# Performance work log

Hardware: AMD Instinct MI355X
Metric: run time of the kernel (lower is better)

## Reference

```python
import jax, jax.numpy as jnp
import numpy as np

N_V = 100000
N_E = 20000
NNZ = 1600000
D = 128


def setup_inputs() -> dict:
    key = jax.random.key(0)
    k1, k2, k3, k4, k5 = jax.random.split(key, 5)
    X = jax.random.normal(k1, (N_V, D), dtype=jnp.float32)
    W = jax.random.normal(k2, (D, D), dtype=jnp.float32) * (1.0 / np.sqrt(D))
    b = jax.random.normal(k3, (D,), dtype=jnp.float32) * 0.01
    v2e_src = jax.random.randint(k4, (NNZ,), 0, N_V, dtype=jnp.int32)
    v2e_dst = jax.random.randint(k5, (NNZ,), 0, N_E, dtype=jnp.int32)
    return {"X": X, "W": W, "b": b, "v2e_src": v2e_src, "v2e_dst": v2e_dst, "num_e": N_E}


def reference(X, W, b, v2e_src, v2e_dst, num_e):
    num_v = X.shape[0]
    ones = jnp.ones(v2e_src.shape[0], dtype=X.dtype)
    # node degrees (values of D_v diagonal) and hyperedge incidence counts
    deg_v = jax.ops.segment_sum(ones, v2e_src, num_segments=num_v)
    cnt_e = jax.ops.segment_sum(ones, v2e_dst, num_segments=num_e)

    # theta: linear layer
    Xt = X @ W.T + b  # [N_V, D]

    # v2e mean aggregation: per hyperedge, mean of incident vertex features
    Ysum = jax.ops.segment_sum(Xt[v2e_src], v2e_dst, num_segments=num_e)  # [N_E, D]
    Y = Ysum / jnp.maximum(cnt_e, 1.0)[:, None]

    # edge norm: torch scatter_reduce(reduce='mean', include_self=True) -> sum/(count+1)
    De_sum = jax.ops.segment_sum(deg_v[v2e_src], v2e_dst, num_segments=num_e)
    De = De_sum / (cnt_e + 1.0)
    De = jnp.where(De > 0, jax.lax.rsqrt(jnp.maximum(De, 1e-30)), 1.0)  # inf -> 1
    Y = De[:, None] * Y

    # e2v sum aggregation
    Xo = jax.ops.segment_sum(Y[v2e_dst], v2e_src, num_segments=num_v)  # [N_V, D]

    # D_v^{-1/2} sparse diagonal mm (zero-degree nodes -> 0)
    dvn = jnp.where(deg_v > 0, jax.lax.rsqrt(jnp.maximum(deg_v, 1e-30)), 0.0)
    Xo = dvn[:, None] * Xo

    # is_last=False: ReLU then dropout (dropout is identity in eval)
    return jax.nn.relu(Xo)
```

## Files before the change

### kernel.cpp

```cpp
#include <hip/hip_runtime.h>
#include <hip/hip_bf16.h>

#define NV 100000
#define NE 20000
#define DD 128
#define ESHIFT 7
#define VSHIFT 9
#define NBE 157
#define NBV 196
#define NBK 256
#define CHUNK 4096
#define CAPE 11264
#define CAPV 9216

using bf16 = __hip_bfloat16;

typedef __attribute__((ext_vector_type(8))) short frag_ab;
typedef __attribute__((ext_vector_type(4))) float frag_cd;

__device__ __forceinline__ float uas(unsigned u) { union { unsigned u; float f; } c; c.u = u; return c.f; }
__device__ __forceinline__ unsigned pk2(float lo, float hi) {
    bf16 l = __float2bfloat16(lo), h = __float2bfloat16(hi);
    return (unsigned)(*(unsigned short*)&l) | ((unsigned)(*(unsigned short*)&h) << 16);
}
__device__ __forceinline__ void accum8(float* a, uint4 x) {
    a[0] += uas(x.x << 16); a[1] += uas(x.x & 0xffff0000u);
    a[2] += uas(x.y << 16); a[3] += uas(x.y & 0xffff0000u);
    a[4] += uas(x.z << 16); a[5] += uas(x.z & 0xffff0000u);
    a[6] += uas(x.w << 16); a[7] += uas(x.w & 0xffff0000u);
}
__device__ __forceinline__ int wave_incl_scan(int v, int lane) {
#pragma unroll
    for (int o = 1; o < 64; o <<= 1) {
        int x = __shfl_up(v, o);
        if (lane >= o) v += x;
    }
    return v;
}

__global__ void init_cur(int* __restrict__ bcur_e, int* __restrict__ bcur_v) {
    int t = threadIdx.x;
    bcur_e[t] = t * CAPE;
    bcur_v[t] = t * CAPV;
}

__global__ __launch_bounds__(256) void partition_and_cvt(const int* __restrict__ src, const int* __restrict__ dst,
                                                         int* __restrict__ bcur_e, int* __restrict__ bcur_v,
                                                         unsigned* __restrict__ pairs_e, unsigned* __restrict__ pairs_v,
                                                         int nnz,
                                                         const float4* __restrict__ Xf, ushort4* __restrict__ Xb,
                                                         const float4* __restrict__ Wf, ushort4* __restrict__ Wb) {
    int nchunk = (nnz + CHUNK - 1) / CHUNK;
    int t = threadIdx.x;
    int bid = blockIdx.x;
    if (bid >= 2 * nchunk) {
        const int n4x = NV * DD / 4;
        const int n4w = DD * DD / 4;
        int i = (bid - 2 * nchunk) * 256 + t;
        if (i < n4x + n4w) {
            float4 v;
            ushort4 o;
            if (i < n4x) v = Xf[i]; else v = Wf[i - n4x];
            bf16 a = __float2bfloat16(v.x); o.x = *(unsigned short*)&a;
            bf16 b = __float2bfloat16(v.y); o.y = *(unsigned short*)&b;
            bf16 c = __float2bfloat16(v.z); o.z = *(unsigned short*)&c;
            bf16 d = __float2bfloat16(v.w); o.w = *(unsigned short*)&d;
            if (i < n4x) Xb[i] = o; else Wb[i - n4x] = o;
        }
        return;
    }
    __shared__ int cntA[NBK], cntB[NBK], pre1[NBK], loff[NBK], gbase[NBK], wsum[4];
    __shared__ int totValid;
    __shared__ unsigned stage[CHUNK];
    int phase = (bid >= nchunk) ? 1 : 0;
    int cidx = phase ? bid - nchunk : bid;
    int sub = t >> 7;
    int lane = t & 63, wv = t >> 6;
    int base = cidx * CHUNK;
    unsigned p[16];
    int rk[16];
#pragma unroll
    for (int k = 0; k < 16; ++k) {
        int i = base + k * 256 + t;
        p[k] = (i < nnz) ? (((unsigned)src[i] << 15) | (unsigned)dst[i]) : 0xFFFFFFFFu;
    }

    cntA[t] = 0; cntB[t] = 0;
    __syncthreads();
#pragma unroll
    for (int k = 0; k < 16; ++k)
        if (p[k] != 0xFFFFFFFFu) {
            int b = phase ? (int)(p[k] >> 24) : (int)((p[k] >> ESHIFT) & 0xFF);
            rk[k] = atomicAdd(sub ? &cntB[b] : &cntA[b], 1);
        }
    __syncthreads();
    {
        int a = cntA[t], bb = cntB[t];
        int tv = a + bb;
        pre1[t] = a;
        int incl = wave_incl_scan(tv, lane);
        if (lane == 63) wsum[wv] = incl;
        __syncthreads();
        if (t == 0) { int r = 0; for (int i = 0; i < 4; ++i) { int x = wsum[i]; wsum[i] = r; r += x; } }
        __syncthreads();
        int ex = incl - tv + wsum[wv];
        loff[t] = ex;
        gbase[t] = (tv > 0) ? atomicAdd(phase ? &bcur_v[t] : &bcur_e[t], tv) : 0;
        if (t == 255) totValid = ex + tv;
    }
    __syncthreads();
#pragma unroll
    for (int k = 0; k < 16; ++k)
        if (p[k] != 0xFFFFFFFFu) {
            int b = phase ? (int)(p[k] >> 24) : (int)((p[k] >> ESHIFT) & 0xFF);
            stage[loff[b] + rk[k] + (sub ? pre1[b] : 0)] = p[k];
        }
    __syncthreads();
    unsigned* outp = phase ? pairs_v : pairs_e;
    for (int i = t; i < totValid; i += 256) {
        unsigned pp = stage[i];
        int b = phase ? (int)(pp >> 24) : (int)((pp >> ESHIFT) & 0xFF);
        outp[gbase[b] + i - loff[b]] = pp;
    }
}

__global__ __launch_bounds__(1024) void build_csr(const unsigned* __restrict__ pairs_e, const int* __restrict__ bcur_e,
                                                  int* __restrict__ off_e, int* __restrict__ end_e, int* __restrict__ e_src,
                                                  const unsigned* __restrict__ pairs_v, const int* __restrict__ bcur_v,
                                                  int* __restrict__ off_v, int* __restrict__ end_v, int* __restrict__ v_edge,
                                                  int* __restrict__ deg_v) {
    __shared__ int cA[2048], cB[2048], sc2[512], eoff[512], wsumS[8];
    int t = threadIdx.x;
    cA[t] = 0; cA[t + 1024] = 0;
    __syncthreads();
    if ((int)blockIdx.x < NBE) {
        int b = blockIdx.x;
        int lo = b * CAPE, hi = bcur_e[b];
        int sub = t >> 7;
        unsigned pv[12];
        int rk[12];
        int kk = 0;
        for (int i = lo + t; i < hi; i += 1024, ++kk) {
            unsigned p = pairs_e[i];
            pv[kk] = p;
            rk[kk] = atomicAdd(&cA[sub * 128 + (p & 127)], 1);
        }
        __syncthreads();
        if (t < 128) {
            int run = 0;
#pragma unroll
            for (int s = 0; s < 8; ++s) { cB[s * 128 + t] = run; run += cA[s * 128 + t]; }
            sc2[t] = run;
        }
        __syncthreads();
        int incl = 0, myrun = 0;
        if (t < 128) {
            myrun = sc2[t];
            incl = wave_incl_scan(myrun, t & 63);
            if ((t & 63) == 63) wsumS[t >> 6] = incl;
        }
        __syncthreads();
        if (t == 0) { int r = 0; for (int i = 0; i < 2; ++i) { int x = wsumS[i]; wsumS[i] = r; r += x; } }
        __syncthreads();
        if (t < 128) {
            int ex = incl - myrun + wsumS[t >> 6];
            eoff[t] = ex;
            int e = (b << ESHIFT) + t;
            if (e < NE) { off_e[e] = lo + ex; end_e[e] = lo + ex + myrun; }
        }
        __syncthreads();
        for (int k = 0; k < kk; ++k) {
            int bkt = pv[k] & 127;
            int pos = lo + eoff[bkt] + cB[sub * 128 + bkt] + rk[k];
            e_src[pos] = (int)(pv[k] >> 15);
        }
    } else {
        int b = blockIdx.x - NBE;
        int lo = b * CAPV, hi = bcur_v[b];
        int sub = t >> 8;
        unsigned pv[9];
        int rk[9];
        int kk = 0;
        for (int i = lo + t; i < hi; i += 1024, ++kk) {
            unsigned p = pairs_v[i];
            pv[kk] = p;
            rk[kk] = atomicAdd(&cA[sub * 512 + ((p >> 15) & 511)], 1);
        }
        __syncthreads();
        if (t < 512) {
            int run = 0;
#pragma unroll
            for (int s = 0; s < 4; ++s) { cB[s * 512 + t] = run; run += cA[s * 512 + t]; }
            sc2[t] = run;
        }
        __syncthreads();
        int incl = 0, myrun = 0;
        if (t < 512) {
            myrun = sc2[t];
            incl = wave_incl_scan(myrun, t & 63);
            if ((t & 63) == 63) wsumS[t >> 6] = incl;
        }
        __syncthreads();
        if (t == 0) { int r = 0; for (int i = 0; i < 8; ++i) { int x = wsumS[i]; wsumS[i] = r; r += x; } }
        __syncthreads();
        if (t < 512) {
            int ex = incl - myrun + wsumS[t >> 6];
            eoff[t] = ex;
            int v = (b << VSHIFT) + t;
            if (v < NV) { off_v[v] = lo + ex; end_v[v] = lo + ex + myrun; deg_v[v] = myrun; }
        }
        __syncthreads();
        for (int k = 0; k < kk; ++k) {
            int bkt = (pv[k] >> 15) & 511;
            int pos = lo + eoff[bkt] + cB[sub * 512 + bkt] + rk[k];
            v_edge[pos] = (int)(pv[k] & 0x7FFF);
        }
    }
}

__global__ __launch_bounds__(512) void edge_fused(const uint4* __restrict__ Xq, const int* __restrict__ off_e,
                                                  const int* __restrict__ end_e,
                                                  const int* __restrict__ e_src, const int* __restrict__ deg_v,
                                                  const bf16* __restrict__ Wb, const float* __restrict__ bias,
                                                  bf16* __restrict__ Y) {
    __shared__ short Stile[16][136];
    __shared__ float betaL[16];
    int t = threadIdx.x;
    int w = t >> 6, lane = t & 63;
    int h = lane >> 5;
    int g2 = (lane >> 4) & 1;
    int l16 = lane & 15;
    int mBase = blockIdx.x * 16;
    int le = w * 2 + g2;
    int e = mBase + le;
    int start = off_e[e], end = end_e[e];
    int cnt = end - start;
    int half0 = (cnt + 1) >> 1;
    int hs = start + h * half0;
    int he = h ? end : (start + half0);
    float acc[8] = {0.f, 0.f, 0.f, 0.f, 0.f, 0.f, 0.f, 0.f};
    float degsum = 0.f;
    int j = hs;
    for (; j + 8 <= he; j += 8) {
        int s0 = e_src[j + 0], s1 = e_src[j + 1], s2 = e_src[j + 2], s3 = e_src[j + 3];
        int s4 = e_src[j + 4], s5 = e_src[j + 5], s6 = e_src[j + 6], s7 = e_src[j + 7];
        uint4 x0 = Xq[(size_t)s0 * 16 + l16];
        uint4 x1 = Xq[(size_t)s1 * 16 + l16];
        uint4 x2 = Xq[(size_t)s2 * 16 + l16];
        uint4 x3 = Xq[(size_t)s3 * 16 + l16];
        uint4 x4 = Xq[(size_t)s4 * 16 + l16];
        uint4 x5 = Xq[(size_t)s5 * 16 + l16];
        uint4 x6 = Xq[(size_t)s6 * 16 + l16];
        uint4 x7 = Xq[(size_t)s7 * 16 + l16];
        degsum += (float)(deg_v[s0] + deg_v[s1] + deg_v[s2] + deg_v[s3]
                        + deg_v[s4] + deg_v[s5] + deg_v[s6] + deg_v[s7]);
        accum8(acc, x0); accum8(acc, x1); accum8(acc, x2); accum8(acc, x3);
        accum8(acc, x4); accum8(acc, x5); accum8(acc, x6); accum8(acc, x7);
    }
    for (; j + 4 <= he; j += 4) {
        int s0 = e_src[j + 0], s1 = e_src[j + 1], s2 = e_src[j + 2], s3 = e_src[j + 3];
        uint4 x0 = Xq[(size_t)s0 * 16 + l16];
        uint4 x1 = Xq[(size_t)s1 * 16 + l16];
        uint4 x2 = Xq[(size_t)s2 * 16 + l16];
        uint4 x3 = Xq[(size_t)s3 * 16 + l16];
        degsum += (float)(deg_v[s0] + deg_v[s1] + deg_v[s2] + deg_v[s3]);
        accum8(acc, x0); accum8(acc, x1); accum8(acc, x2); accum8(acc, x3);
    }
    for (; j < he; ++j) {
        int s = e_src[j];
        uint4 x = Xq[(size_t)s * 16 + l16];
        degsum += (float)deg_v[s];
        accum8(acc, x);
    }
#pragma unroll
    for (int r = 0; r < 8; ++r) acc[r] += __shfl_xor(acc[r], 32);
    degsum += __shfl_xor(degsum, 32);

    float cntf = (float)cnt;
    float Des = degsum / (cntf + 1.0f);
    float De = (Des > 0.f) ? rsqrtf(fmaxf(Des, 1e-30f)) : 1.0f;
    float scale = De / fmaxf(cntf, 1.0f);
    if (h == 0) {
        uint4 o;
        o.x = pk2(acc[0] * scale, acc[1] * scale);
        o.y = pk2(acc[2] * scale, acc[3] * scale);
        o.z = pk2(acc[4] * scale, acc[5] * scale);
        o.w = pk2(acc[6] * scale, acc[7] * scale);
        *(uint4*)&Stile[le][l16 * 8] = o;
        if (l16 == 0) betaL[le] = (cntf > 0.f) ? De : 0.f;
    }
    __syncthreads();

    const short* Ws = (const short*)Wb;
    int quad = lane >> 4;
    frag_ab a[4];
#pragma unroll
    for (int kt = 0; kt < 4; ++kt)
        a[kt] = *(const frag_ab*)&Stile[l16][kt * 32 + quad * 8];
    float beta_r[4];
#pragma unroll
    for (int r = 0; r < 4; ++r) beta_r[r] = betaL[quad * 4 + r];

    int nt = w;
    frag_cd acc2 = {0.f, 0.f, 0.f, 0.f};
#pragma unroll
    for (int kt = 0; kt < 4; ++kt) {
        frag_ab bfr = *(const frag_ab*)(Ws + (size_t)(nt * 16 + l16) * DD + kt * 32 + quad * 8);
        acc2 = __builtin_amdgcn_mfma_f32_16x16x32_bf16(a[kt], bfr, acc2, 0, 0, 0);
    }
    float bv = bias[nt * 16 + l16];
#pragma unroll
    for (int r = 0; r < 4; ++r) {
        int row = mBase + quad * 4 + r;
        float v = acc2[r] + beta_r[r] * bv;
        Y[(size_t)row * DD + nt * 16 + l16] = __float2bfloat16(v);
    }
}

__global__ __launch_bounds__(256) void vertex_agg(const uint4* __restrict__ Yq, const int* __restrict__ off_v,
                                                  const int* __restrict__ end_v,
                                                  const int* __restrict__ v_edge, float* __restrict__ out) {
    int wave = (blockIdx.x * blockDim.x + threadIdx.x) >> 6;
    int lane = threadIdx.x & 63;
    int g = lane >> 4, l16 = lane & 15;
    int v = wave * 4 + g;
    if (v >= NV) return;
    int start = off_v[v], end = end_v[v];
    float acc[8] = {0.f, 0.f, 0.f, 0.f, 0.f, 0.f, 0.f, 0.f};
    int j = start;
    for (; j + 8 <= end; j += 8) {
        int e0 = v_edge[j + 0], e1 = v_edge[j + 1], e2 = v_edge[j + 2], e3 = v_edge[j + 3];
        int e4 = v_edge[j + 4], e5 = v_edge[j + 5], e6 = v_edge[j + 6], e7 = v_edge[j + 7];
        uint4 y0 = Yq[(size_t)e0 * 16 + l16];
        uint4 y1 = Yq[(size_t)e1 * 16 + l16];
        uint4 y2 = Yq[(size_t)e2 * 16 + l16];
        uint4 y3 = Yq[(size_t)e3 * 16 + l16];
        uint4 y4 = Yq[(size_t)e4 * 16 + l16];
        uint4 y5 = Yq[(size_t)e5 * 16 + l16];
        uint4 y6 = Yq[(size_t)e6 * 16 + l16];
        uint4 y7 = Yq[(size_t)e7 * 16 + l16];
        accum8(acc, y0); accum8(acc, y1); accum8(acc, y2); accum8(acc, y3);
        accum8(acc, y4); accum8(acc, y5); accum8(acc, y6); accum8(acc, y7);
    }
    for (; j + 4 <= end; j += 4) {
        int e0 = v_edge[j + 0], e1 = v_edge[j + 1], e2 = v_edge[j + 2], e3 = v_edge[j + 3];
        uint4 y0 = Yq[(size_t)e0 * 16 + l16];
        uint4 y1 = Yq[(size_t)e1 * 16 + l16];
        uint4 y2 = Yq[(size_t)e2 * 16 + l16];
        uint4 y3 = Yq[(size_t)e3 * 16 + l16];
        accum8(acc, y0); accum8(acc, y1); accum8(acc, y2); accum8(acc, y3);
    }
    for (; j < end; ++j) {
        int e = v_edge[j];
        uint4 y = Yq[(size_t)e * 16 + l16];
        accum8(acc, y);
    }
    int deg = end - start;
    float dvn = (deg > 0) ? rsqrtf((float)deg) : 0.f;
    float4 o1, o2;
    o1.x = fmaxf(acc[0] * dvn, 0.f);
    o1.y = fmaxf(acc[1] * dvn, 0.f);
    o1.z = fmaxf(acc[2] * dvn, 0.f);
    o1.w = fmaxf(acc[3] * dvn, 0.f);
    o2.x = fmaxf(acc[4] * dvn, 0.f);
    o2.y = fmaxf(acc[5] * dvn, 0.f);
    o2.z = fmaxf(acc[6] * dvn, 0.f);
    o2.w = fmaxf(acc[7] * dvn, 0.f);
    float4* op = (float4*)(out + (size_t)v * DD + l16 * 8);
    op[0] = o1;
    op[1] = o2;
}

extern "C" void kernel_launch(void* const* d_in, const int* in_sizes, int n_in,
                              void* d_out, int out_size, void* d_ws, size_t ws_size,
                              hipStream_t stream) {
    const float* X = (const float*)d_in[0];
    const float* W = (const float*)d_in[1];
    const float* b = (const float*)d_in[2];
    const int* src = (const int*)d_in[3];
    const int* dst = (const int*)d_in[4];
    int nnz = in_sizes[3];

    char* ws = (char*)d_ws;
    size_t o = 0;
    auto take = [&](size_t bytes) -> char* {
        char* p = ws + o;
        o += (bytes + 255) & ~(size_t)255;
        return p;
    };
    int* bcur_e = (int*)take(NBK * 4);
    int* bcur_v = (int*)take(NBK * 4);
    int* off_e = (int*)take((size_t)NE * 4);
    int* end_e = (int*)take((size_t)NE * 4);
    int* off_v = (int*)take((size_t)NV * 4);
    int* end_v = (int*)take((size_t)NV * 4);
    int* deg_v = (int*)take((size_t)NV * 4);
    int* e_src = (int*)take((size_t)NBE * CAPE * 4);
    int* v_edge = (int*)take((size_t)NBV * CAPV * 4);
    unsigned* pairs_e = (unsigned*)take((size_t)NBE * CAPE * 4);
    unsigned* pairs_v = (unsigned*)take((size_t)NBV * CAPV * 4);
    bf16* Y = (bf16*)take((size_t)NE * DD * 2);
    bf16* Wb = (bf16*)take((size_t)DD * DD * 2);
    bf16* Xb = (bf16*)take((size_t)NV * DD * 2);
    (void)ws_size; (void)n_in; (void)out_size;

    int nchunk = (nnz + CHUNK - 1) / CHUNK;
    int ncvt = (NV * DD / 4 + DD * DD / 4 + 255) / 256;

    init_cur<<<1, NBK, 0, stream>>>(bcur_e, bcur_v);
    partition_and_cvt<<<2 * nchunk + ncvt, 256, 0, stream>>>(src, dst, bcur_e, bcur_v, pairs_e, pairs_v, nnz,
                                                             (const float4*)X, (ushort4*)Xb,
                                                             (const float4*)W, (ushort4*)Wb);
    build_csr<<<NBE + NBV, 1024, 0, stream>>>(pairs_e, bcur_e, off_e, end_e, e_src,
                                              pairs_v, bcur_v, off_v, end_v, v_edge, deg_v);
    edge_fused<<<NE / 16, 512, 0, stream>>>((const uint4*)Xb, off_e, end_e, e_src, deg_v, Wb, b, Y);
    vertex_agg<<<(NV / 4 * 64) / 256, 256, 0, stream>>>((const uint4*)Y, off_v, end_v, v_edge, (float*)d_out);
}
```

Before: 248.8 us.

## Fuse edge-side CSR sort into edge kernel via finer buckets and LDS local sort

Edges are now partitioned into 1250 buckets of 16 hyperedges. Each edge_fused block sorts its own bucket in LDS and aggregates directly from that list, so the separate edge half of build_csr and the global e_src array go away. The vertex sort becomes a standalone vsort kernel with 256-vertex buckets that stores edge indices as 16-bit values and drops end arrays. The trade-offs are a larger partition histogram, fixed per-bucket capacity limits that could overflow on other inputs, and one 16-lane group per edge without the old split-half parallelism.

```diff
diff --git a/kernel.cpp b/kernel.cpp
--- a/kernel.cpp
+++ b/kernel.cpp
@@ -4,14 +4,14 @@
 #define NV 100000
 #define NE 20000
 #define DD 128
-#define ESHIFT 7
-#define VSHIFT 9
-#define NBE 157
-#define NBV 196
-#define NBK 256
+#define NBE 1250
+#define NBV 391
+#define NBMAX 1280
+#define PBE 5
+#define PBV 2
 #define CHUNK 4096
-#define CAPE 11264
-#define CAPV 9216
+#define CAPE 1664
+#define CAPV 5120
 
 using bf16 = __hip_bfloat16;
 
@@ -40,8 +40,8 @@
 
 __global__ void init_cur(int* __restrict__ bcur_e, int* __restrict__ bcur_v) {
     int t = threadIdx.x;
-    bcur_e[t] = t * CAPE;
-    bcur_v[t] = t * CAPV;
+    for (int i = t; i < NBE; i += 1024) bcur_e[i] = i * CAPE;
+    for (int i = t; i < NBV; i += 1024) bcur_v[i] = i * CAPV;
 }
 
 __global__ __launch_bounds__(256) void partition_and_cvt(const int* __restrict__ src, const int* __restrict__ dst,
@@ -69,11 +69,14 @@
         }
         return;
     }
-    __shared__ int cntA[NBK], cntB[NBK], pre1[NBK], loff[NBK], gbase[NBK], wsum[4];
+    __shared__ int cntA[NBMAX], cntB[NBMAX], loff[NBMAX], gbase[NBMAX], wsum[4];
     __shared__ int totValid;
     __shared__ unsigned stage[CHUNK];
     int phase = (bid >= nchunk) ? 1 : 0;
     int cidx = phase ? bid - nchunk : bid;
+    int NB = phase ? NBV : NBE;
+    int PB = phase ? PBV : PBE;
+    int* cur = phase ? bcur_v : bcur_e;
     int sub = t >> 7;
     int lane = t & 63, wv = t >> 6;
     int base = cidx * CHUNK;
@@ -85,165 +88,161 @@
         p[k] = (i < nnz) ? (((unsigned)src[i] << 15) | (unsigned)dst[i]) : 0xFFFFFFFFu;
     }
 
-    cntA[t] = 0; cntB[t] = 0;
+    for (int i = t; i < NBMAX; i += 256) { cntA[i] = 0; cntB[i] = 0; }
     __syncthreads();
 #pragma unroll
     for (int k = 0; k < 16; ++k)
         if (p[k] != 0xFFFFFFFFu) {
-            int b = phase ? (int)(p[k] >> 24) : (int)((p[k] >> ESHIFT) & 0xFF);
+            int b = phase ? (int)(p[k] >> 23) : (int)((p[k] >> 4) & 0x7FF);
             rk[k] = atomicAdd(sub ? &cntB[b] : &cntA[b], 1);
         }
     __syncthreads();
     {
-        int a = cntA[t], bb = cntB[t];
-        int tv = a + bb;
-        pre1[t] = a;
-        int incl = wave_incl_scan(tv, lane);
+        int run = 0;
+        int lcl[PBE];
+#pragma unroll
+        for (int q = 0; q < PBE; ++q) lcl[q] = 0;
+        for (int q = 0; q < PB; ++q) {
+            int bkt = t * PB + q;
+            int tv = (bkt < NB) ? (cntA[bkt] + cntB[bkt]) : 0;
+            lcl[q] = run; run += tv;
+        }
+        int incl = wave_incl_scan(run, lane);
         if (lane == 63) wsum[wv] = incl;
         __syncthreads();
         if (t == 0) { int r = 0; for (int i = 0; i < 4; ++i) { int x = wsum[i]; wsum[i] = r; r += x; } }
         __syncthreads();
-        int ex = incl - tv + wsum[wv];
-        loff[t] = ex;
-        gbase[t] = (tv > 0) ? atomicAdd(phase ? &bcur_v[t] : &bcur_e[t], tv) : 0;
-        if (t == 255) totValid = ex + tv;
+        int ex = incl - run + wsum[wv];
+        for (int q = 0; q < PB; ++q) {
+            int bkt = t * PB + q;
+            if (bkt < NB) {
+                int tv = cntA[bkt] + cntB[bkt];
+                loff[bkt] = ex + lcl[q];
+                gbase[bkt] = (tv > 0) ? atomicAdd(&cur[bkt], tv) : 0;
+            }
+        }
+        if (t == 255) totValid = ex + run;
     }
     __syncthreads();
 #pragma unroll
     for (int k = 0; k < 16; ++k)
         if (p[k] != 0xFFFFFFFFu) {
-            int b = phase ? (int)(p[k] >> 24) : (int)((p[k] >> ESHIFT) & 0xFF);
-            stage[loff[b] + rk[k] + (sub ? pre1[b] : 0)] = p[k];
+            int b = phase ? (int)(p[k] >> 23) : (int)((p[k] >> 4) & 0x7FF);
+            stage[loff[b] + rk[k] + (sub ? cntA[b] : 0)] = p[k];
         }
     __syncthreads();
     unsigned* outp = phase ? pairs_v : pairs_e;
     for (int i = t; i < totValid; i += 256) {
         unsigned pp = stage[i];
-        int b = phase ? (int)(pp >> 24) : (int)((pp >> ESHIFT) & 0xFF);
+        int b = phase ? (int)(pp >> 23) : (int)((pp >> 4) & 0x7FF);
         outp[gbase[b] + i - loff[b]] = pp;
     }
 }
 
-__global__ __launch_bounds__(1024) void build_csr(const unsigned* __restrict__ pairs_e, const int* __restrict__ bcur_e,
-                                                  int* __restrict__ off_e, int* __restrict__ end_e, int* __restrict__ e_src,
-                                                  const unsigned* __restrict__ pairs_v, const int* __restrict__ bcur_v,
-                                                  int* __restrict__ off_v, int* __restrict__ end_v, int* __restrict__ v_edge,
-                                                  int* __restrict__ deg_v) {
-    __shared__ int cA[2048], cB[2048], sc2[512], eoff[512], wsumS[8];
+__global__ __launch_bounds__(1024) void vsort(const unsigned* __restrict__ pairs_v, const int* __restrict__ bcur_v,
+                                              int* __restrict__ off_v, int* __restrict__ deg_v,
+                                              unsigned short* __restrict__ v_edge) {
+    __shared__ int cA[1024], cB[1024], sc2[256], eoff[256], wsumS[4];
     int t = threadIdx.x;
-    cA[t] = 0; cA[t + 1024] = 0;
-    __syncthreads();
-    if ((int)blockIdx.x < NBE) {
-        int b = blockIdx.x;
-        int lo = b * CAPE, hi = bcur_e[b];
-        int sub = t >> 7;
-        unsigned pv[12];
-        int rk[12];
-        int kk = 0;
-        for (int i = lo + t; i < hi; i += 1024, ++kk) {
-            unsigned p = pairs_e[i];
-            pv[kk] = p;
-            rk[kk] = atomicAdd(&cA[sub * 128 + (p & 127)], 1);
-        }
-        __syncthreads();
-        if (t < 128) {
-            int run = 0;
-#pragma unroll
-            for (int s = 0; s < 8; ++s) { cB[s * 128 + t] = run; run += cA[s * 128 + t]; }
-            sc2[t] = run;
-        }
-        __syncthreads();
-        int incl = 0, myrun = 0;
-        if (t < 128) {
-            myrun = sc2[t];
-            incl = wave_incl_scan(myrun, t & 63);
-            if ((t & 63) == 63) wsumS[t >> 6] = incl;
-        }
-        __syncthreads();
-        if (t == 0) { int r = 0; for (int i = 0; i < 2; ++i) { int x = wsumS[i]; wsumS[i] = r; r += x; } }
-        __syncthreads();
-        if (t < 128) {
-            int ex = incl - myrun + wsumS[t >> 6];
-            eoff[t] = ex;
-            int e = (b << ESHIFT) + t;
-            if (e < NE) { off_e[e] = lo + ex; end_e[e] = lo + ex + myrun; }
-        }
-        __syncthreads();
-        for (int k = 0; k < kk; ++k) {
-            int bkt = pv[k] & 127;
-            int pos = lo + eoff[bkt] + cB[sub * 128 + bkt] + rk[k];
-            e_src[pos] = (int)(pv[k] >> 15);
-        }
-    } else {
-        int b = blockIdx.x - NBE;
-        int lo = b * CAPV, hi = bcur_v[b];
-        int sub = t >> 8;
-        unsigned pv[9];
-        int rk[9];
-        int kk = 0;
-        for (int i = lo + t; i < hi; i += 1024, ++kk) {
-            unsigned p = pairs_v[i];
-            pv[kk] = p;
-            rk[kk] = atomicAdd(&cA[sub * 512 + ((p >> 15) & 511)], 1);
-        }
-        __syncthreads();
-        if (t < 512) {
-            int run = 0;
-#pragma unroll
-            for (int s = 0; s < 4; ++s) { cB[s * 512 + t] = run; run += cA[s * 512 + t]; }
-            sc2[t] = run;
-        }
-        __syncthreads();
-        int incl = 0, myrun = 0;
-        if (t < 512) {
-            myrun = sc2[t];
-            incl = wave_incl_scan(myrun, t & 63);
-            if ((t & 63) == 63) wsumS[t >> 6] = incl;
-        }
-        __syncthreads();
-        if (t == 0) { int r = 0; for (int i = 0; i < 8; ++i) { int x = wsumS[i]; wsumS[i] = r; r += x; } }
-        __syncthreads();
-        if (t < 512) {
-            int ex = incl - myrun + wsumS[t >> 6];
-            eoff[t] = ex;
-            int v = (b << VSHIFT) + t;
-            if (v < NV) { off_v[v] = lo + ex; end_v[v] = lo + ex + myrun; deg_v[v] = myrun; }
-        }
-        __syncthreads();
-        for (int k = 0; k < kk; ++k) {
-            int bkt = (pv[k] >> 15) & 511;
-            int pos = lo + eoff[bkt] + cB[sub * 512 + bkt] + rk[k];
-            v_edge[pos] = (int)(pv[k] & 0x7FFF);
-        }
-    }
-}
-
-__global__ __launch_bounds__(512) void edge_fused(const uint4* __restrict__ Xq, const int* __restrict__ off_e,
-                                                  const int* __restrict__ end_e,
-                                                  const int* __restrict__ e_src, const int* __restrict__ deg_v,
+    cA[t] = 0;
+    __syncthreads();
+    int b = blockIdx.x;
+    int lo = b * CAPV, hi = bcur_v[b];
+    int sub = t >> 8;
+    unsigned pv[5];
+    int rk[5];
+    int kk = 0;
+    for (int i = lo + t; i < hi; i += 1024, ++kk) {
+        unsigned p = pairs_v[i];
+        pv[kk] = p;
+        rk[kk] = atomicAdd(&cA[sub * 256 + ((p >> 15) & 255)], 1);
+    }
+    __syncthreads();
+    if (t < 256) {
+        int run = 0;
+#pragma unroll
+        for (int s = 0; s < 4; ++s) { cB[s * 256 + t] = run; run += cA[s * 256 + t]; }
+        sc2[t] = run;
+    }
+    __syncthreads();
+    int incl = 0, myrun = 0;
+    if (t < 256) {
+        myrun = sc2[t];
+        incl = wave_incl_scan(myrun, t & 63);
+        if ((t & 63) == 63) wsumS[t >> 6] = incl;
+    }
+    __syncthreads();
+    if (t == 0) { int r = 0; for (int i = 0; i < 4; ++i) { int x = wsumS[i]; wsumS[i] = r; r += x; } }
+    __syncthreads();
+    if (t < 256) {
+        int ex = incl - myrun + wsumS[t >> 6];
+        eoff[t] = ex;
+        int v = (b << 8) + t;
+        if (v < NV) { off_v[v] = lo + ex; deg_v[v] = myrun; }
+    }
+    __syncthreads();
+    for (int k = 0; k < kk; ++k) {
+        int bkt = (pv[k] >> 15) & 255;
+        int pos = lo + eoff[bkt] + cB[sub * 256 + bkt] + rk[k];
+        v_edge[pos] = (unsigned short)(pv[k] & 0x7FFF);
+    }
+}
+
+__global__ __launch_bounds__(256) void edge_fused(const uint4* __restrict__ Xq, const unsigned* __restrict__ pairs_e,
+                                                  const int* __restrict__ bcur_e, const int* __restrict__ deg_v,
                                                   const bf16* __restrict__ Wb, const float* __restrict__ bias,
                                                   bf16* __restrict__ Y) {
+    __shared__ int cntS[64], cB16[64], cntE[16], eoffS[16];
+    __shared__ int Lst[CAPE];
     __shared__ short Stile[16][136];
     __shared__ float betaL[16];
     int t = threadIdx.x;
     int w = t >> 6, lane = t & 63;
-    int h = lane >> 5;
-    int g2 = (lane >> 4) & 1;
-    int l16 = lane & 15;
-    int mBase = blockIdx.x * 16;
-    int le = w * 2 + g2;
-    int e = mBase + le;
-    int start = off_e[e], end = end_e[e];
-    int cnt = end - start;
-    int half0 = (cnt + 1) >> 1;
-    int hs = start + h * half0;
-    int he = h ? end : (start + half0);
+    int g = lane >> 4, l16 = lane & 15;
+    int bkt = blockIdx.x;
+    int lo = bkt * CAPE, hi = bcur_e[bkt];
+    int sub = w;
+
+    if (t < 64) cntS[t] = 0;
+    __syncthreads();
+    unsigned pv[7];
+    int rk[7];
+    int kk = 0;
+    for (int i = lo + t; i < hi; i += 256, ++kk) {
+        unsigned p = pairs_e[i];
+        pv[kk] = p;
+        rk[kk] = atomicAdd(&cntS[sub * 16 + (p & 15)], 1);
+    }
+    __syncthreads();
+    if (t < 16) {
+        int run = 0;
+#pragma unroll
+        for (int s = 0; s < 4; ++s) { cB16[s * 16 + t] = run; run += cntS[s * 16 + t]; }
+        cntE[t] = run;
+    }
+    __syncthreads();
+    if (w == 0) {
+        int v = (lane < 16) ? cntE[lane] : 0;
+        int incl = wave_incl_scan(v, lane);
+        if (lane < 16) eoffS[lane] = incl - v;
+    }
+    __syncthreads();
+    for (int k = 0; k < kk; ++k) {
+        int bb = pv[k] & 15;
+        Lst[eoffS[bb] + cB16[sub * 16 + bb] + rk[k]] = (int)(pv[k] >> 15);
+    }
+    __syncthreads();
+
+    int mBase = bkt * 16;
+    int le = t >> 4;
+    int start = eoffS[le], cnt = cntE[le];
+    int end = start + cnt;
     float acc[8] = {0.f, 0.f, 0.f, 0.f, 0.f, 0.f, 0.f, 0.f};
     float degsum = 0.f;
-    int j = hs;
-    for (; j + 8 <= he; j += 8) {
-        int s0 = e_src[j + 0], s1 = e_src[j + 1], s2 = e_src[j + 2], s3 = e_src[j + 3];
-        int s4 = e_src[j + 4], s5 = e_src[j + 5], s6 = e_src[j + 6], s7 = e_src[j + 7];
+    int j = start;
+    for (; j + 8 <= end; j += 8) {
+        int s0 = Lst[j + 0], s1 = Lst[j + 1], s2 = Lst[j + 2], s3 = Lst[j + 3];
+        int s4 = Lst[j + 4], s5 = Lst[j + 5], s6 = Lst[j + 6], s7 = Lst[j + 7];
         uint4 x0 = Xq[(size_t)s0 * 16 + l16];
         uint4 x1 = Xq[(size_t)s1 * 16 + l16];
         uint4 x2 = Xq[(size_t)s2 * 16 + l16];
@@ -257,8 +256,8 @@
         accum8(acc, x0); accum8(acc, x1); accum8(acc, x2); accum8(acc, x3);
         accum8(acc, x4); accum8(acc, x5); accum8(acc, x6); accum8(acc, x7);
     }
-    for (; j + 4 <= he; j += 4) {
-        int s0 = e_src[j + 0], s1 = e_src[j + 1], s2 = e_src[j + 2], s3 = e_src[j + 3];
+    for (; j + 4 <= end; j += 4) {
+        int s0 = Lst[j + 0], s1 = Lst[j + 1], s2 = Lst[j + 2], s3 = Lst[j + 3];
         uint4 x0 = Xq[(size_t)s0 * 16 + l16];
         uint4 x1 = Xq[(size_t)s1 * 16 + l16];
         uint4 x2 = Xq[(size_t)s2 * 16 + l16];
@@ -266,21 +265,17 @@
         degsum += (float)(deg_v[s0] + deg_v[s1] + deg_v[s2] + deg_v[s3]);
         accum8(acc, x0); accum8(acc, x1); accum8(acc, x2); accum8(acc, x3);
     }
-    for (; j < he; ++j) {
-        int s = e_src[j];
+    for (; j < end; ++j) {
+        int s = Lst[j];
         uint4 x = Xq[(size_t)s * 16 + l16];
         degsum += (float)deg_v[s];
         accum8(acc, x);
     }
-#pragma unroll
-    for (int r = 0; r < 8; ++r) acc[r] += __shfl_xor(acc[r], 32);
-    degsum += __shfl_xor(degsum, 32);
-
     float cntf = (float)cnt;
     float Des = degsum / (cntf + 1.0f);
     float De = (Des > 0.f) ? rsqrtf(fmaxf(Des, 1e-30f)) : 1.0f;
     float scale = De / fmaxf(cntf, 1.0f);
-    if (h == 0) {
+    {
         uint4 o;
         o.x = pk2(acc[0] * scale, acc[1] * scale);
         o.y = pk2(acc[2] * scale, acc[3] * scale);
@@ -292,7 +287,7 @@
     __syncthreads();
 
     const short* Ws = (const short*)Wb;
-    int quad = lane >> 4;
+    int quad = g;
     frag_ab a[4];
 #pragma unroll
     for (int kt = 0; kt < 4; ++kt)
@@ -301,31 +296,35 @@
 #pragma unroll
     for (int r = 0; r < 4; ++r) beta_r[r] = betaL[quad * 4 + r];
 
-    int nt = w;
-    frag_cd acc2 = {0.f, 0.f, 0.f, 0.f};
-#pragma unroll
-    for (int kt = 0; kt < 4; ++kt) {
-        frag_ab bfr = *(const frag_ab*)(Ws + (size_t)(nt * 16 + l16) * DD + kt * 32 + quad * 8);
-        acc2 = __builtin_amdgcn_mfma_f32_16x16x32_bf16(a[kt], bfr, acc2, 0, 0, 0);
-    }
-    float bv = bias[nt * 16 + l16];
-#pragma unroll
-    for (int r = 0; r < 4; ++r) {
-        int row = mBase + quad * 4 + r;
-        float v = acc2[r] + beta_r[r] * bv;
-        Y[(size_t)row * DD + nt * 16 + l16] = __float2bfloat16(v);
+#pragma unroll
+    for (int nn = 0; nn < 2; ++nn) {
+        int nt = w * 2 + nn;
+        frag_cd acc2 = {0.f, 0.f, 0.f, 0.f};
+#pragma unroll
+        for (int kt = 0; kt < 4; ++kt) {
+            frag_ab bfr = *(const frag_ab*)(Ws + (size_t)(nt * 16 + l16) * DD + kt * 32 + quad * 8);
+            acc2 = __builtin_amdgcn_mfma_f32_16x16x32_bf16(a[kt], bfr, acc2, 0, 0, 0);
+        }
+        float bv = bias[nt * 16 + l16];
+#pragma unroll
+        for (int r = 0; r < 4; ++r) {
+            int row = mBase + quad * 4 + r;
+            float v = acc2[r] + beta_r[r] * bv;
+            Y[(size_t)row * DD + nt * 16 + l16] = __float2bfloat16(v);
+        }
     }
 }
 
 __global__ __launch_bounds__(256) void vertex_agg(const uint4* __restrict__ Yq, const int* __restrict__ off_v,
-                                                  const int* __restrict__ end_v,
-                                                  const int* __restrict__ v_edge, float* __restrict__ out) {
+                                                  const int* __restrict__ deg_v,
+                                                  const unsigned short* __restrict__ v_edge, float* __restrict__ out) {
     int wave = (blockIdx.x * blockDim.x + threadIdx.x) >> 6;
     int lane = threadIdx.x & 63;
     int g = lane >> 4, l16 = lane & 15;
     int v = wave * 4 + g;
     if (v >= NV) return;
-    int start = off_v[v], end = end_v[v];
+    int start = off_v[v], deg = deg_v[v];
+    int end = start + deg;
     float acc[8] = {0.f, 0.f, 0.f, 0.f, 0.f, 0.f, 0.f, 0.f};
     int j = start;
     for (; j + 8 <= end; j += 8) {
@@ -355,7 +354,6 @@
         uint4 y = Yq[(size_t)e * 16 + l16];
         accum8(acc, y);
     }
-    int deg = end - start;
     float dvn = (deg > 0) ? rsqrtf((float)deg) : 0.f;
     float4 o1, o2;
     o1.x = fmaxf(acc[0] * dvn, 0.f);
@@ -388,15 +386,11 @@
         o += (bytes + 255) & ~(size_t)255;
         return p;
     };
-    int* bcur_e = (int*)take(NBK * 4);
-    int* bcur_v = (int*)take(NBK * 4);
-    int* off_e = (int*)take((size_t)NE * 4);
-    int* end_e = (int*)take((size_t)NE * 4);
+    int* bcur_e = (int*)take((size_t)NBE * 4);
+    int* bcur_v = (int*)take((size_t)NBV * 4);
     int* off_v = (int*)take((size_t)NV * 4);
-    int* end_v = (int*)take((size_t)NV * 4);
     int* deg_v = (int*)take((size_t)NV * 4);
-    int* e_src = (int*)take((size_t)NBE * CAPE * 4);
-    int* v_edge = (int*)take((size_t)NBV * CAPV * 4);
+    unsigned short* v_edge = (unsigned short*)take((size_t)NBV * CAPV * 2);
     unsigned* pairs_e = (unsigned*)take((size_t)NBE * CAPE * 4);
     unsigned* pairs_v = (unsigned*)take((size_t)NBV * CAPV * 4);
     bf16* Y = (bf16*)take((size_t)NE * DD * 2);
@@ -407,12 +401,11 @@
     int nchunk = (nnz + CHUNK - 1) / CHUNK;
     int ncvt = (NV * DD / 4 + DD * DD / 4 + 255) / 256;
 
-    init_cur<<<1, NBK, 0, stream>>>(bcur_e, bcur_v);
+    init_cur<<<1, 1024, 0, stream>>>(bcur_e, bcur_v);
     partition_and_cvt<<<2 * nchunk + ncvt, 256, 0, stream>>>(src, dst, bcur_e, bcur_v, pairs_e, pairs_v, nnz,
                                                              (const float4*)X, (ushort4*)Xb,
                                                              (const float4*)W, (ushort4*)Wb);
-    build_csr<<<NBE + NBV, 1024, 0, stream>>>(pairs_e, bcur_e, off_e, end_e, e_src,
-                                              pairs_v, bcur_v, off_v, end_v, v_edge, deg_v);
-    edge_fused<<<NE / 16, 512, 0, stream>>>((const uint4*)Xb, off_e, end_e, e_src, deg_v, Wb, b, Y);
-    vertex_agg<<<(NV / 4 * 64) / 256, 256, 0, stream>>>((const uint4*)Y, off_v, end_v, v_edge, (float*)d_out);
-}
+    vsort<<<NBV, 1024, 0, stream>>>(pairs_v, bcur_v, off_v, deg_v, v_edge);
+    edge_fused<<<NBE, 256, 0, stream>>>((const uint4*)Xb, pairs_e, bcur_e, deg_v, Wb, b, Y);
+    vertex_agg<<<(NV / 4 * 64) / 256, 256, 0, stream>>>((const uint4*)Y, off_v, deg_v, v_edge, (float*)d_out);
+}
```

New measurement: 279.8 us. 12.5% more time.

## Split vertex aggregation into two column halves and shrink edge-list indices to 16-bit

Applied to the files above, without the earlier changes.

The vertex aggregation is split into two launches, each gathering one 64-column half of Y. Each half of Y (about 2.5 MB) is more likely to stay resident in L2 or the MI355X's last-level cache during the random gathers. The per-vertex edge list becomes unsigned short, and end_v is replaced by deg_v, which cuts index traffic. The init kernel is replaced by a memset plus relative bucket offsets. The trade-off is that the index list and offsets are read twice and each gather is narrower (8-byte loads instead of 16-byte).

```diff
diff --git a/kernel.cpp b/kernel.cpp
--- a/kernel.cpp
+++ b/kernel.cpp
@@ -29,6 +29,10 @@
     a[4] += uas(x.z << 16); a[5] += uas(x.z & 0xffff0000u);
     a[6] += uas(x.w << 16); a[7] += uas(x.w & 0xffff0000u);
 }
+__device__ __forceinline__ void accum4(float* a, uint2 x) {
+    a[0] += uas(x.x << 16); a[1] += uas(x.x & 0xffff0000u);
+    a[2] += uas(x.y << 16); a[3] += uas(x.y & 0xffff0000u);
+}
 __device__ __forceinline__ int wave_incl_scan(int v, int lane) {
 #pragma unroll
     for (int o = 1; o < 64; o <<= 1) {
@@ -36,12 +40,6 @@
         if (lane >= o) v += x;
     }
     return v;
-}
-
-__global__ void init_cur(int* __restrict__ bcur_e, int* __restrict__ bcur_v) {
-    int t = threadIdx.x;
-    bcur_e[t] = t * CAPE;
-    bcur_v[t] = t * CAPV;
 }
 
 __global__ __launch_bounds__(256) void partition_and_cvt(const int* __restrict__ src, const int* __restrict__ dst,
@@ -105,7 +103,8 @@
         __syncthreads();
         int ex = incl - tv + wsum[wv];
         loff[t] = ex;
-        gbase[t] = (tv > 0) ? atomicAdd(phase ? &bcur_v[t] : &bcur_e[t], tv) : 0;
+        int rel = (tv > 0) ? atomicAdd(phase ? &bcur_v[t] : &bcur_e[t], tv) : 0;
+        gbase[t] = t * (phase ? CAPV : CAPE) + rel;
         if (t == 255) totValid = ex + tv;
     }
     __syncthreads();
@@ -127,7 +126,7 @@
 __global__ __launch_bounds__(1024) void build_csr(const unsigned* __restrict__ pairs_e, const int* __restrict__ bcur_e,
                                                   int* __restrict__ off_e, int* __restrict__ end_e, int* __restrict__ e_src,
                                                   const unsigned* __restrict__ pairs_v, const int* __restrict__ bcur_v,
-                                                  int* __restrict__ off_v, int* __restrict__ end_v, int* __restrict__ v_edge,
+                                                  int* __restrict__ off_v, unsigned short* __restrict__ v_edge,
                                                   int* __restrict__ deg_v) {
     __shared__ int cA[2048], cB[2048], sc2[512], eoff[512], wsumS[8];
     int t = threadIdx.x;
@@ -135,7 +134,7 @@
     __syncthreads();
     if ((int)blockIdx.x < NBE) {
         int b = blockIdx.x;
-        int lo = b * CAPE, hi = bcur_e[b];
+        int lo = b * CAPE, hi = lo + bcur_e[b];
         int sub = t >> 7;
         unsigned pv[12];
         int rk[12];
@@ -176,7 +175,7 @@
         }
     } else {
         int b = blockIdx.x - NBE;
-        int lo = b * CAPV, hi = bcur_v[b];
+        int lo = b * CAPV, hi = lo + bcur_v[b];
         int sub = t >> 8;
         unsigned pv[9];
         int rk[9];
@@ -207,13 +206,13 @@
             int ex = incl - myrun + wsumS[t >> 6];
             eoff[t] = ex;
             int v = (b << VSHIFT) + t;
-            if (v < NV) { off_v[v] = lo + ex; end_v[v] = lo + ex + myrun; deg_v[v] = myrun; }
+            if (v < NV) { off_v[v] = lo + ex; deg_v[v] = myrun; }
         }
         __syncthreads();
         for (int k = 0; k < kk; ++k) {
             int bkt = (pv[k] >> 15) & 511;
             int pos = lo + eoff[bkt] + cB[sub * 512 + bkt] + rk[k];
-            v_edge[pos] = (int)(pv[k] & 0x7FFF);
+            v_edge[pos] = (unsigned short)(pv[k] & 0x7FFF);
         }
     }
 }
@@ -317,58 +316,54 @@
     }
 }
 
-__global__ __launch_bounds__(256) void vertex_agg(const uint4* __restrict__ Yq, const int* __restrict__ off_v,
-                                                  const int* __restrict__ end_v,
-                                                  const int* __restrict__ v_edge, float* __restrict__ out) {
+__global__ __launch_bounds__(256) void vertex_agg(const uint2* __restrict__ Yq, const int* __restrict__ off_v,
+                                                  const int* __restrict__ deg_v,
+                                                  const unsigned short* __restrict__ v_edge, float* __restrict__ out,
+                                                  int half) {
     int wave = (blockIdx.x * blockDim.x + threadIdx.x) >> 6;
     int lane = threadIdx.x & 63;
     int g = lane >> 4, l16 = lane & 15;
     int v = wave * 4 + g;
     if (v >= NV) return;
-    int start = off_v[v], end = end_v[v];
-    float acc[8] = {0.f, 0.f, 0.f, 0.f, 0.f, 0.f, 0.f, 0.f};
+    int start = off_v[v], deg = deg_v[v];
+    int end = start + deg;
+    const uint2* Yh = Yq + half * 16 + l16;
+    float acc[4] = {0.f, 0.f, 0.f, 0.f};
     int j = start;
     for (; j + 8 <= end; j += 8) {
         int e0 = v_edge[j + 0], e1 = v_edge[j + 1], e2 = v_edge[j + 2], e3 = v_edge[j + 3];
         int e4 = v_edge[j + 4], e5 = v_edge[j + 5], e6 = v_edge[j + 6], e7 = v_edge[j + 7];
-        uint4 y0 = Yq[(size_t)e0 * 16 + l16];
-        uint4 y1 = Yq[(size_t)e1 * 16 + l16];
-        uint4 y2 = Yq[(size_t)e2 * 16 + l16];
-        uint4 y3 = Yq[(size_t)e3 * 16 + l16];
-        uint4 y4 = Yq[(size_t)e4 * 16 + l16];
-        uint4 y5 = Yq[(size_t)e5 * 16 + l16];
-        uint4 y6 = Yq[(size_t)e6 * 16 + l16];
-        uint4 y7 = Yq[(size_t)e7 * 16 + l16];
-        accum8(acc, y0); accum8(acc, y1); accum8(acc, y2); accum8(acc, y3);
-        accum8(acc, y4); accum8(acc, y5); accum8(acc, y6); accum8(acc, y7);
+        uint2 y0 = Yh[(size_t)e0 * 32];
+        uint2 y1 = Yh[(size_t)e1 * 32];
+        uint2 y2 = Yh[(size_t)e2 * 32];
+        uint2 y3 = Yh[(size_t)e3 * 32];
+        uint2 y4 = Yh[(size_t)e4 * 32];
+        uint2 y5 = Yh[(size_t)e5 * 32];
+        uint2 y6 = Yh[(size_t)e6 * 32];
+        uint2 y7 = Yh[(size_t)e7 * 32];
+        accum4(acc, y0); accum4(acc, y1); accum4(acc, y2); accum4(acc, y3);
+        accum4(acc, y4); accum4(acc, y5); accum4(acc, y6); accum4(acc, y7);
     }
     for (; j + 4 <= end; j += 4) {
         int e0 = v_edge[j + 0], e1 = v_edge[j + 1], e2 = v_edge[j + 2], e3 = v_edge[j + 3];
-        uint4 y0 = Yq[(size_t)e0 * 16 + l16];
-        uint4 y1 = Yq[(size_t)e1 * 16 + l16];
-        uint4 y2 = Yq[(size_t)e2 * 16 + l16];
-        uint4 y3 = Yq[(size_t)e3 * 16 + l16];
-        accum8(acc, y0); accum8(acc, y1); accum8(acc, y2); accum8(acc, y3);
+        uint2 y0 = Yh[(size_t)e0 * 32];
+        uint2 y1 = Yh[(size_t)e1 * 32];
+        uint2 y2 = Yh[(size_t)e2 * 32];
+        uint2 y3 = Yh[(size_t)e3 * 32];
+        accum4(acc, y0); accum4(acc, y1); accum4(acc, y2); accum4(acc, y3);
     }
     for (; j < end; ++j) {
         int e = v_edge[j];
-        uint4 y = Yq[(size_t)e * 16 + l16];
-        accum8(acc, y);
-    }
-    int deg = end - start;
+        uint2 y = Yh[(size_t)e * 32];
+        accum4(acc, y);
+    }
     float dvn = (deg > 0) ? rsqrtf((float)deg) : 0.f;
-    float4 o1, o2;
+    float4 o1;
     o1.x = fmaxf(acc[0] * dvn, 0.f);
     o1.y = fmaxf(acc[1] * dvn, 0.f);
     o1.z = fmaxf(acc[2] * dvn, 0.f);
     o1.w = fmaxf(acc[3] * dvn, 0.f);
-    o2.x = fmaxf(acc[4] * dvn, 0.f);
-    o2.y = fmaxf(acc[5] * dvn, 0.f);
-    o2.z = fmaxf(acc[6] * dvn, 0.f);
-    o2.w = fmaxf(acc[7] * dvn, 0.f);
-    float4* op = (float4*)(out + (size_t)v * DD + l16 * 8);
-    op[0] = o1;
-    op[1] = o2;
+    *(float4*)(out + (size_t)v * DD + half * 64 + l16 * 4) = o1;
 }
 
 extern "C" void kernel_launch(void* const* d_in, const int* in_sizes, int n_in,
@@ -388,15 +383,14 @@
         o += (bytes + 255) & ~(size_t)255;
         return p;
     };
-    int* bcur_e = (int*)take(NBK * 4);
-    int* bcur_v = (int*)take(NBK * 4);
+    int* bcur_e = (int*)take((size_t)2 * NBK * 4);
+    int* bcur_v = bcur_e + NBK;
     int* off_e = (int*)take((size_t)NE * 4);
     int* end_e = (int*)take((size_t)NE * 4);
     int* off_v = (int*)take((size_t)NV * 4);
-    int* end_v = (int*)take((size_t)NV * 4);
     int* deg_v = (int*)take((size_t)NV * 4);
     int* e_src = (int*)take((size_t)NBE * CAPE * 4);
-    int* v_edge = (int*)take((size_t)NBV * CAPV * 4);
+    unsigned short* v_edge = (unsigned short*)take((size_t)NBV * CAPV * 2);
     unsigned* pairs_e = (unsigned*)take((size_t)NBE * CAPE * 4);
     unsigned* pairs_v = (unsigned*)take((size_t)NBV * CAPV * 4);
     bf16* Y = (bf16*)take((size_t)NE * DD * 2);
@@ -407,12 +401,13 @@
     int nchunk = (nnz + CHUNK - 1) / CHUNK;
     int ncvt = (NV * DD / 4 + DD * DD / 4 + 255) / 256;
 
-    init_cur<<<1, NBK, 0, stream>>>(bcur_e, bcur_v);
+    hipMemsetAsync(bcur_e, 0, (size_t)2 * NBK * 4, stream);
     partition_and_cvt<<<2 * nchunk + ncvt, 256, 0, stream>>>(src, dst, bcur_e, bcur_v, pairs_e, pairs_v, nnz,
                                                              (const float4*)X, (ushort4*)Xb,
                                                              (const float4*)W, (ushort4*)Wb);
     build_csr<<<NBE + NBV, 1024, 0, stream>>>(pairs_e, bcur_e, off_e, end_e, e_src,
-                                              pairs_v, bcur_v, off_v, end_v, v_edge, deg_v);
+                                              pairs_v, bcur_v, off_v, v_edge, deg_v);
     edge_fused<<<NE / 16, 512, 0, stream>>>((const uint4*)Xb, off_e, end_e, e_src, deg_v, Wb, b, Y);
-    vertex_agg<<<(NV / 4 * 64) / 256, 256, 0, stream>>>((const uint4*)Y, off_v, end_v, v_edge, (float*)d_out);
-}
+    vertex_agg<<<NV / 16, 256, 0, stream>>>((const uint2*)Y, off_v, deg_v, v_edge, (float*)d_out, 0);
+    vertex_agg<<<NV / 16, 256, 0, stream>>>((const uint2*)Y, off_v, deg_v, v_edge, (float*)d_out, 1);
+}
```

Measured after the change: 262.9 us. 5.7% more time.

## Shrink vertex CSR to 16-bit edge ids, drop end_v and init kernel

Applied to the files above, without the earlier changes.

The partition kernel now runs 512-thread blocks over 8192-entry chunks, halving the number of partition blocks. The bucket-cursor init kernel is replaced by a memset, with cursors stored relative to each bucket base. The vertex-side CSR stores edge ids as 16-bit values and derives the end index from deg_v instead of a separate end_v array. This cuts index bandwidth in vertex_agg and build_csr and removes one launch, at the cost of a larger per-block shared stage and different occupancy in the partition kernel.

```diff
diff --git a/kernel.cpp b/kernel.cpp
--- a/kernel.cpp
+++ b/kernel.cpp
@@ -9,7 +9,8 @@
 #define NBE 157
 #define NBV 196
 #define NBK 256
-#define CHUNK 4096
+#define CHUNK 8192
+#define PTHREADS 512
 #define CAPE 11264
 #define CAPV 9216
 
@@ -38,25 +39,19 @@
     return v;
 }
 
-__global__ void init_cur(int* __restrict__ bcur_e, int* __restrict__ bcur_v) {
-    int t = threadIdx.x;
-    bcur_e[t] = t * CAPE;
-    bcur_v[t] = t * CAPV;
-}
-
-__global__ __launch_bounds__(256) void partition_and_cvt(const int* __restrict__ src, const int* __restrict__ dst,
-                                                         int* __restrict__ bcur_e, int* __restrict__ bcur_v,
-                                                         unsigned* __restrict__ pairs_e, unsigned* __restrict__ pairs_v,
-                                                         int nnz,
-                                                         const float4* __restrict__ Xf, ushort4* __restrict__ Xb,
-                                                         const float4* __restrict__ Wf, ushort4* __restrict__ Wb) {
+__global__ __launch_bounds__(PTHREADS) void partition_and_cvt(const int* __restrict__ src, const int* __restrict__ dst,
+                                                              int* __restrict__ bcur_e, int* __restrict__ bcur_v,
+                                                              unsigned* __restrict__ pairs_e, unsigned* __restrict__ pairs_v,
+                                                              int nnz,
+                                                              const float4* __restrict__ Xf, ushort4* __restrict__ Xb,
+                                                              const float4* __restrict__ Wf, ushort4* __restrict__ Wb) {
     int nchunk = (nnz + CHUNK - 1) / CHUNK;
     int t = threadIdx.x;
     int bid = blockIdx.x;
     if (bid >= 2 * nchunk) {
         const int n4x = NV * DD / 4;
         const int n4w = DD * DD / 4;
-        int i = (bid - 2 * nchunk) * 256 + t;
+        int i = (bid - 2 * nchunk) * PTHREADS + t;
         if (i < n4x + n4w) {
             float4 v;
             ushort4 o;
@@ -74,18 +69,18 @@
     __shared__ unsigned stage[CHUNK];
     int phase = (bid >= nchunk) ? 1 : 0;
     int cidx = phase ? bid - nchunk : bid;
-    int sub = t >> 7;
-    int lane = t & 63, wv = t >> 6;
+    int sub = t >> 8;
+    int lane = t & 63;
     int base = cidx * CHUNK;
     unsigned p[16];
     int rk[16];
 #pragma unroll
     for (int k = 0; k < 16; ++k) {
-        int i = base + k * 256 + t;
+        int i = base + k * PTHREADS + t;
         p[k] = (i < nnz) ? (((unsigned)src[i] << 15) | (unsigned)dst[i]) : 0xFFFFFFFFu;
     }
 
-    cntA[t] = 0; cntB[t] = 0;
+    if (t < NBK) { cntA[t] = 0; cntB[t] = 0; }
     __syncthreads();
 #pragma unroll
     for (int k = 0; k < 16; ++k)
@@ -95,18 +90,24 @@
         }
     __syncthreads();
     {
-        int a = cntA[t], bb = cntB[t];
-        int tv = a + bb;
-        pre1[t] = a;
-        int incl = wave_incl_scan(tv, lane);
-        if (lane == 63) wsum[wv] = incl;
+        int incl = 0, tv = 0;
+        if (t < NBK) {
+            int a = cntA[t], bb = cntB[t];
+            tv = a + bb;
+            pre1[t] = a;
+            incl = wave_incl_scan(tv, lane);
+            if (lane == 63) wsum[t >> 6] = incl;
+        }
         __syncthreads();
         if (t == 0) { int r = 0; for (int i = 0; i < 4; ++i) { int x = wsum[i]; wsum[i] = r; r += x; } }
         __syncthreads();
-        int ex = incl - tv + wsum[wv];
-        loff[t] = ex;
-        gbase[t] = (tv > 0) ? atomicAdd(phase ? &bcur_v[t] : &bcur_e[t], tv) : 0;
-        if (t == 255) totValid = ex + tv;
+        if (t < NBK) {
+            int ex = incl - tv + wsum[t >> 6];
+            loff[t] = ex;
+            int rel = (tv > 0) ? atomicAdd(phase ? &bcur_v[t] : &bcur_e[t], tv) : 0;
+            gbase[t] = t * (phase ? CAPV : CAPE) + rel;
+            if (t == NBK - 1) totValid = ex + tv;
+        }
     }
     __syncthreads();
 #pragma unroll
@@ -117,7 +118,7 @@
         }
     __syncthreads();
     unsigned* outp = phase ? pairs_v : pairs_e;
-    for (int i = t; i < totValid; i += 256) {
+    for (int i = t; i < totValid; i += PTHREADS) {
         unsigned pp = stage[i];
         int b = phase ? (int)(pp >> 24) : (int)((pp >> ESHIFT) & 0xFF);
         outp[gbase[b] + i - loff[b]] = pp;
@@ -127,7 +128,7 @@
 __global__ __launch_bounds__(1024) void build_csr(const unsigned* __restrict__ pairs_e, const int* __restrict__ bcur_e,
                                                   int* __restrict__ off_e, int* __restrict__ end_e, int* __restrict__ e_src,
                                                   const unsigned* __restrict__ pairs_v, const int* __restrict__ bcur_v,
-                                                  int* __restrict__ off_v, int* __restrict__ end_v, int* __restrict__ v_edge,
+                                                  int* __restrict__ off_v, unsigned short* __restrict__ v_edge,
                                                   int* __restrict__ deg_v) {
     __shared__ int cA[2048], cB[2048], sc2[512], eoff[512], wsumS[8];
     int t = threadIdx.x;
@@ -135,7 +136,7 @@
     __syncthreads();
     if ((int)blockIdx.x < NBE) {
         int b = blockIdx.x;
-        int lo = b * CAPE, hi = bcur_e[b];
+        int lo = b * CAPE, hi = lo + bcur_e[b];
         int sub = t >> 7;
         unsigned pv[12];
         int rk[12];
@@ -176,7 +177,7 @@
         }
     } else {
         int b = blockIdx.x - NBE;
-        int lo = b * CAPV, hi = bcur_v[b];
+        int lo = b * CAPV, hi = lo + bcur_v[b];
         int sub = t >> 8;
         unsigned pv[9];
         int rk[9];
@@ -207,13 +208,13 @@
             int ex = incl - myrun + wsumS[t >> 6];
             eoff[t] = ex;
             int v = (b << VSHIFT) + t;
-            if (v < NV) { off_v[v] = lo + ex; end_v[v] = lo + ex + myrun; deg_v[v] = myrun; }
+            if (v < NV) { off_v[v] = lo + ex; deg_v[v] = myrun; }
         }
         __syncthreads();
         for (int k = 0; k < kk; ++k) {
             int bkt = (pv[k] >> 15) & 511;
             int pos = lo + eoff[bkt] + cB[sub * 512 + bkt] + rk[k];
-            v_edge[pos] = (int)(pv[k] & 0x7FFF);
+            v_edge[pos] = (unsigned short)(pv[k] & 0x7FFF);
         }
     }
 }
@@ -318,14 +319,15 @@
 }
 
 __global__ __launch_bounds__(256) void vertex_agg(const uint4* __restrict__ Yq, const int* __restrict__ off_v,
-                                                  const int* __restrict__ end_v,
-                                                  const int* __restrict__ v_edge, float* __restrict__ out) {
+                                                  const int* __restrict__ deg_v,
+                                                  const unsigned short* __restrict__ v_edge, float* __restrict__ out) {
     int wave = (blockIdx.x * blockDim.x + threadIdx.x) >> 6;
     int lane = threadIdx.x & 63;
     int g = lane >> 4, l16 = lane & 15;
     int v = wave * 4 + g;
     if (v >= NV) return;
-    int start = off_v[v], end = end_v[v];
+    int start = off_v[v], deg = deg_v[v];
+    int end = start + deg;
     float acc[8] = {0.f, 0.f, 0.f, 0.f, 0.f, 0.f, 0.f, 0.f};
     int j = start;
     for (; j + 8 <= end; j += 8) {
@@ -355,7 +357,6 @@
         uint4 y = Yq[(size_t)e * 16 + l16];
         accum8(acc, y);
     }
-    int deg = end - start;
     float dvn = (deg > 0) ? rsqrtf((float)deg) : 0.f;
     float4 o1, o2;
     o1.x = fmaxf(acc[0] * dvn, 0.f);
@@ -388,15 +389,14 @@
         o += (bytes + 255) & ~(size_t)255;
         return p;
     };
-    int* bcur_e = (int*)take(NBK * 4);
-    int* bcur_v = (int*)take(NBK * 4);
+    int* bcur_e = (int*)take((size_t)2 * NBK * 4);
+    int* bcur_v = bcur_e + NBK;
     int* off_e = (int*)take((size_t)NE * 4);
     int* end_e = (int*)take((size_t)NE * 4);
     int* off_v = (int*)take((size_t)NV * 4);
-    int* end_v = (int*)take((size_t)NV * 4);
     int* deg_v = (int*)take((size_t)NV * 4);
     int* e_src = (int*)take((size_t)NBE * CAPE * 4);
-    int* v_edge = (int*)take((size_t)NBV * CAPV * 4);
+    unsigned short* v_edge = (unsigned short*)take((size_t)NBV * CAPV * 2);
     unsigned* pairs_e = (unsigned*)take((size_t)NBE * CAPE * 4);
     unsigned* pairs_v = (unsigned*)take((size_t)NBV * CAPV * 4);
     bf16* Y = (bf16*)take((size_t)NE * DD * 2);
@@ -405,14 +405,14 @@
     (void)ws_size; (void)n_in; (void)out_size;
 
     int nchunk = (nnz + CHUNK - 1) / CHUNK;
-    int ncvt = (NV * DD / 4 + DD * DD / 4 + 255) / 256;
-
-    init_cur<<<1, NBK, 0, stream>>>(bcur_e, bcur_v);
-    partition_and_cvt<<<2 * nchunk + ncvt, 256, 0, stream>>>(src, dst, bcur_e, bcur_v, pairs_e, pairs_v, nnz,
-                                                             (const float4*)X, (ushort4*)Xb,
-                                                             (const float4*)W, (ushort4*)Wb);
+    int ncvt = (NV * DD / 4 + DD * DD / 4 + PTHREADS - 1) / PTHREADS;
+
+    hipMemsetAsync(bcur_e, 0, (size_t)2 * NBK * 4, stream);
+    partition_and_cvt<<<2 * nchunk + ncvt, PTHREADS, 0, stream>>>(src, dst, bcur_e, bcur_v, pairs_e, pairs_v, nnz,
+                                                                  (const float4*)X, (ushort4*)Xb,
+                                                                  (const float4*)W, (ushort4*)Wb);
     build_csr<<<NBE + NBV, 1024, 0, stream>>>(pairs_e, bcur_e, off_e, end_e, e_src,
-                                              pairs_v, bcur_v, off_v, end_v, v_edge, deg_v);
+                                              pairs_v, bcur_v, off_v, v_edge, deg_v);
     edge_fused<<<NE / 16, 512, 0, stream>>>((const uint4*)Xb, off_e, end_e, e_src, deg_v, Wb, b, Y);
-    vertex_agg<<<(NV / 4 * 64) / 256, 256, 0, stream>>>((const uint4*)Y, off_v, end_v, v_edge, (float*)d_out);
-}
+    vertex_agg<<<(NV / 4 * 64) / 256, 256, 0, stream>>>((const uint4*)Y, off_v, deg_v, v_edge, (float*)d_out);
+}
```

After: 241.4 us, median of 2. 1.03x faster.
